# Kernel tuning notes

Measured on AMD Instinct MI355X. Metric: run time of the kernel, lower is better.

Reference implementation:

```python
import jax, jax.numpy as jnp
import numpy as np

NUM_LEVELS = 3
NUM_EMBEDDINGS = 1024
EMBEDDING_DIM = 128
COMMITMENT_COST = 0.25
N_TOKENS = 262144


def setup_inputs() -> dict:
    key = jax.random.key(0)
    k1, k2 = jax.random.split(key)
    z_e = jax.random.normal(k1, (N_TOKENS, EMBEDDING_DIM), dtype=jnp.float32)
    codebooks = jax.random.normal(k2, (NUM_LEVELS, NUM_EMBEDDINGS, EMBEDDING_DIM), dtype=jnp.float32)
    return {"z_e": z_e, "codebooks": codebooks}


def _rvq_forward(z_e, codebooks):
    """Sequential residual VQ: per level cdist + argmin + gather + residual update.

    Per-level losses follow the standard EMA-VQ formulation:
      vq_loss     = mean((z_q - sg(residual))^2)
      commit_loss = beta * mean((sg(z_q) - residual)^2)
    with straight-through estimator z_q_st = residual + sg(z_q - residual).
    """
    sg = jax.lax.stop_gradient
    residual = z_e
    z_q_total = jnp.zeros_like(z_e)
    all_indices = []
    vq_loss = jnp.float32(0.0)
    commit_loss = jnp.float32(0.0)
    num_levels = codebooks.shape[0]
    for lvl in range(num_levels):  # small fixed loop over levels (sequential by design)
        E = codebooks[lvl]  # [K, D]
        # squared-distance matrix [N, K]: ||r||^2 + ||e||^2 - 2 r.e
        d = (jnp.sum(residual * residual, axis=1, keepdims=True)
             + jnp.sum(E * E, axis=1)
             - 2.0 * (residual @ E.T))
        idx = jnp.argmin(d, axis=1)           # [N]
        z_q = E[idx]                           # gather [N, D]
        vq_loss = vq_loss + jnp.mean((z_q - sg(residual)) ** 2)
        commit_loss = commit_loss + COMMITMENT_COST * jnp.mean((sg(z_q) - residual) ** 2)
        z_q_st = residual + sg(z_q - residual)  # straight-through
        z_q_total = z_q_total + z_q_st
        residual = residual - z_q_st
        all_indices.append(idx)
    L = jnp.float32(num_levels)
    stacked_indices = jnp.stack(all_indices, axis=1)  # [N, num_levels]
    return z_q_total, vq_loss / L, commit_loss / L, stacked_indices


def reference(z_e, codebooks):
    return _rvq_forward(z_e, codebooks)
```

## Files before the change

### kernel.cpp

```cpp
#include <hip/hip_runtime.h>
#include <math.h>

#define N_TOK   262144
#define DIMV    128
#define KCODE   1024
#define LEV     3
#define BLOCK   256
#define NTILES  64
#define EPS     0.08f

#define WS_EE64_B  64
#define WS_EE32_B  24640
#define WS_FRAG_B  36928

typedef _Float16 f16x8 __attribute__((ext_vector_type(8)));
typedef float f32x4 __attribute__((ext_vector_type(4)));

__global__ void rvq_prep(const float* __restrict__ cb, double* __restrict__ ws) {
    int c = blockIdx.x * blockDim.x + threadIdx.x;
    if (c == 0) ws[0] = 0.0;
    if (c >= LEV * KCODE) return;
    const float* e = cb + (size_t)c * DIMV;
    const int lvl = c >> 10, ci = c & 1023, t4 = ci >> 4, n = ci & 15;
    unsigned char* fb = (unsigned char*)ws + WS_FRAG_B + (((size_t)(lvl * 64 + t4)) << 12);
    double s = 0.0;
    #pragma unroll
    for (int st = 0; st < 4; ++st)
        #pragma unroll
        for (int kq = 0; kq < 4; ++kq) {
            float4 a = *(const float4*)(e + st*32 + kq*8);
            float4 b = *(const float4*)(e + st*32 + kq*8 + 4);
            f16x8 h;
            h[0]=(_Float16)a.x; h[1]=(_Float16)a.y; h[2]=(_Float16)a.z; h[3]=(_Float16)a.w;
            h[4]=(_Float16)b.x; h[5]=(_Float16)b.y; h[6]=(_Float16)b.z; h[7]=(_Float16)b.w;
            s = fma((double)a.x,(double)a.x,s); s = fma((double)a.y,(double)a.y,s);
            s = fma((double)a.z,(double)a.z,s); s = fma((double)a.w,(double)a.w,s);
            s = fma((double)b.x,(double)b.x,s); s = fma((double)b.y,(double)b.y,s);
            s = fma((double)b.z,(double)b.z,s); s = fma((double)b.w,(double)b.w,s);
            *(f16x8*)(fb + st*1024 + ((kq*16 + n) << 4)) = h;
        }
    ((double*)((unsigned char*)ws + WS_EE64_B))[c] = s;
    ((float*)((unsigned char*)ws + WS_EE32_B))[c] = (float)(s + 8192.0);
}

__device__ inline unsigned sel4(const unsigned v[4], int j) {
    unsigned a = (j & 1) ? v[1] : v[0];
    unsigned b = (j & 1) ? v[3] : v[2];
    return (j & 2) ? b : a;
}

__global__ __launch_bounds__(BLOCK, 2) void rvq_main(const float* __restrict__ ze,
                                                     const float* __restrict__ cb,
                                                     float* __restrict__ out,
                                                     double* __restrict__ ws) {
    __shared__ double ssum[4];

    const double* __restrict__ ee64g = (const double*)((const unsigned char*)ws + WS_EE64_B);
    const float*  __restrict__ eebg  = (const float*)((const unsigned char*)ws + WS_EE32_B);
    const unsigned char* __restrict__ fbase = (const unsigned char*)ws + WS_FRAG_B;

    const int tid  = threadIdx.x;
    const int lane = tid & 63;
    const int wid  = tid >> 6;
    const int q    = lane >> 4;
    const int col  = lane & 15;
    const long tokbase = (long)blockIdx.x * 128 + wid * 32;

    float r[2][4][8];
    f16x8 Ah[2][4], Al[2][4];

    #pragma unroll
    for (int mt = 0; mt < 2; ++mt) {
        const float4* zp = (const float4*)(ze + (size_t)(tokbase + mt*16 + col) * DIMV);
        #pragma unroll
        for (int st = 0; st < 4; ++st) {
            float4 a = zp[st*8 + q*2], b = zp[st*8 + q*2 + 1];
            r[mt][st][0]=a.x; r[mt][st][1]=a.y; r[mt][st][2]=a.z; r[mt][st][3]=a.w;
            r[mt][st][4]=b.x; r[mt][st][5]=b.y; r[mt][st][6]=b.z; r[mt][st][7]=b.w;
        }
    }
    #pragma unroll
    for (int mt = 0; mt < 2; ++mt)
        #pragma unroll
        for (int st = 0; st < 4; ++st) {
            f16x8 h, lo;
            #pragma unroll
            for (int j = 0; j < 8; ++j) {
                float y = -2.0f * r[mt][st][j];
                _Float16 hh = (_Float16)y;
                h[j] = hh;
                lo[j] = (_Float16)(y - (float)hh);
            }
            Ah[mt][st] = h; Al[mt][st] = lo;
        }

    double loss = 0.0;
    float* out_idx = out + (size_t)N_TOK * DIMV + 2;

#define TILE_COMPUTE(B, EEQ, T)                                                      \
    do {                                                                             \
        f32x4 c0  = {(EEQ),(EEQ),(EEQ),(EEQ)};                                       \
        f32x4 c1v = {(EEQ),(EEQ),(EEQ),(EEQ)};                                       \
        c0  = __builtin_amdgcn_mfma_f32_16x16x32_f16(Ah[0][0], (B)[0], c0,  0,0,0);  \
        c1v = __builtin_amdgcn_mfma_f32_16x16x32_f16(Ah[1][0], (B)[0], c1v, 0,0,0);  \
        c0  = __builtin_amdgcn_mfma_f32_16x16x32_f16(Al[0][0], (B)[0], c0,  0,0,0);  \
        c1v = __builtin_amdgcn_mfma_f32_16x16x32_f16(Al[1][0], (B)[0], c1v, 0,0,0);  \
        c0  = __builtin_amdgcn_mfma_f32_16x16x32_f16(Ah[0][1], (B)[1], c0,  0,0,0);  \
        c1v = __builtin_amdgcn_mfma_f32_16x16x32_f16(Ah[1][1], (B)[1], c1v, 0,0,0);  \
        c0  = __builtin_amdgcn_mfma_f32_16x16x32_f16(Al[0][1], (B)[1], c0,  0,0,0);  \
        c1v = __builtin_amdgcn_mfma_f32_16x16x32_f16(Al[1][1], (B)[1], c1v, 0,0,0);  \
        c0  = __builtin_amdgcn_mfma_f32_16x16x32_f16(Ah[0][2], (B)[2], c0,  0,0,0);  \
        c1v = __builtin_amdgcn_mfma_f32_16x16x32_f16(Ah[1][2], (B)[2], c1v, 0,0,0);  \
        c0  = __builtin_amdgcn_mfma_f32_16x16x32_f16(Al[0][2], (B)[2], c0,  0,0,0);  \
        c1v = __builtin_amdgcn_mfma_f32_16x16x32_f16(Al[1][2], (B)[2], c1v, 0,0,0);  \
        c0  = __builtin_amdgcn_mfma_f32_16x16x32_f16(Ah[0][3], (B)[3], c0,  0,0,0);  \
        c1v = __builtin_amdgcn_mfma_f32_16x16x32_f16(Ah[1][3], (B)[3], c1v, 0,0,0);  \
        c0  = __builtin_amdgcn_mfma_f32_16x16x32_f16(Al[0][3], (B)[3], c0,  0,0,0);  \
        c1v = __builtin_amdgcn_mfma_f32_16x16x32_f16(Al[1][3], (B)[3], c1v, 0,0,0);  \
        _Pragma("unroll")                                                            \
        for (int i = 0; i < 4; ++i) {                                                \
            unsigned k0 = (__float_as_uint(c0[i]) << 6) | (unsigned)(T);             \
            m2[0][i] = min(m2[0][i], max(m1[0][i], k0));                             \
            m1[0][i] = min(m1[0][i], k0);                                            \
            unsigned k1_ = (__float_as_uint(c1v[i]) << 6) | (unsigned)(T);           \
            m2[1][i] = min(m2[1][i], max(m1[1][i], k1_));                            \
            m1[1][i] = min(m1[1][i], k1_);                                           \
        }                                                                            \
    } while (0)

    for (int l = 0; l < LEV; ++l) {
        const unsigned char* bp = fbase + ((size_t)l << 18) + (lane << 4);
        const float* eep = eebg + l * KCODE + col;

        f16x8 Ba[4], Bb[4];
        #pragma unroll
        for (int st = 0; st < 4; ++st) Ba[st] = *(const f16x8*)(bp + st*1024);
        float eeq_a = eep[0], eeq_b;

        unsigned m1[2][4], m2[2][4];
        #pragma unroll
        for (int mt = 0; mt < 2; ++mt)
            #pragma unroll
            for (int i = 0; i < 4; ++i) { m1[mt][i] = 0xFFFFFFFFu; m2[mt][i] = 0xFFFFFFFFu; }

        for (int t = 0; t < NTILES; t += 2) {
            {
                const unsigned char* np = bp + 4096;
                #pragma unroll
                for (int st = 0; st < 4; ++st) Bb[st] = *(const f16x8*)(np + st*1024);
                eeq_b = eep[16];
            }
            TILE_COMPUTE(Ba, eeq_a, t);
            {
                const unsigned char* np = (t + 2 < NTILES) ? bp + 8192 : bp;
                const float* ep2 = (t + 2 < NTILES) ? eep + 32 : eep;
                #pragma unroll
                for (int st = 0; st < 4; ++st) Ba[st] = *(const f16x8*)(np + st*1024);
                eeq_a = ep2[0];
            }
            TILE_COMPUTE(Bb, eeq_b, t + 1);
            bp += 8192; eep += 32;
        }

        unsigned k1[2][4], k2[2][4], q1[2][4], q2[2][4];
        #pragma unroll
        for (int mt = 0; mt < 2; ++mt)
            #pragma unroll
            for (int i = 0; i < 4; ++i) {
                k1[mt][i] = m1[mt][i]; k2[mt][i] = m2[mt][i];
                q1[mt][i] = (unsigned)col; q2[mt][i] = (unsigned)col;
            }
        #pragma unroll
        for (int d = 1; d <= 8; d <<= 1) {
            #pragma unroll
            for (int mt = 0; mt < 2; ++mt)
                #pragma unroll
                for (int i = 0; i < 4; ++i) {
                    unsigned ok1 = __shfl_xor(k1[mt][i], d), oq1 = __shfl_xor(q1[mt][i], d);
                    unsigned ok2 = __shfl_xor(k2[mt][i], d), oq2 = __shfl_xor(q2[mt][i], d);
                    bool sw = (ok1 < k1[mt][i]) || (ok1 == k1[mt][i] && oq1 < q1[mt][i]);
                    unsigned n1 = sw ? ok1 : k1[mt][i], nq1 = sw ? oq1 : q1[mt][i];
                    unsigned hk = sw ? k1[mt][i] : ok1, hq = sw ? q1[mt][i] : oq1;
                    bool s2 = (ok2 < k2[mt][i]) || (ok2 == k2[mt][i] && oq2 < q2[mt][i]);
                    unsigned p2 = s2 ? ok2 : k2[mt][i], pq = s2 ? oq2 : q2[mt][i];
                    bool s3 = (p2 < hk) || (p2 == hk && pq < hq);
                    k1[mt][i] = n1;              q1[mt][i] = nq1;
                    k2[mt][i] = s3 ? p2 : hk;    q2[mt][i] = s3 ? pq : hq;
                }
        }

        int jsel = (lane >> 2) & 3;
        int S = ((col >> 2) << 4) | ((col & 3) << 2);

        #pragma unroll
        for (int mt = 0; mt < 2; ++mt) {
            unsigned sk1 = sel4(k1[mt], jsel), sq1 = sel4(q1[mt], jsel);
            unsigned sk2 = sel4(k2[mt], jsel), sq2 = sel4(q2[mt], jsel);
            unsigned bk1 = (unsigned)__shfl((int)sk1, S);
            unsigned bq1 = (unsigned)__shfl((int)sq1, S);
            unsigned bk2 = (unsigned)__shfl((int)sk2, S);
            unsigned bq2 = (unsigned)__shfl((int)sq2, S);
            int c1c = (int)(((bk1 & 63u) << 4) | bq1);
            int c2c = (int)(((bk2 & 63u) << 4) | bq2);
            float d1 = __uint_as_float((bk1 >> 6) | 0x44000000u) - 8192.0f;
            float d2 = __uint_as_float((bk2 >> 6) | 0x44000000u) - 8192.0f;
            int bc = c1c;
            if (d2 - d1 < EPS) {
                double s1 = 0.0, s2d = 0.0;
                const float4* e1 = (const float4*)(cb + ((size_t)l*KCODE + c1c)*DIMV);
                const float4* e2 = (const float4*)(cb + ((size_t)l*KCODE + c2c)*DIMV);
                #pragma unroll
                for (int st = 0; st < 4; ++st) {
                    float4 a = e1[st*8 + q*2], b = e1[st*8 + q*2 + 1];
                    s1 = fma((double)a.x,(double)r[mt][st][0],s1); s1 = fma((double)a.y,(double)r[mt][st][1],s1);
                    s1 = fma((double)a.z,(double)r[mt][st][2],s1); s1 = fma((double)a.w,(double)r[mt][st][3],s1);
                    s1 = fma((double)b.x,(double)r[mt][st][4],s1); s1 = fma((double)b.y,(double)r[mt][st][5],s1);
                    s1 = fma((double)b.z,(double)r[mt][st][6],s1); s1 = fma((double)b.w,(double)r[mt][st][7],s1);
                    float4 a2 = e2[st*8 + q*2], b2 = e2[st*8 + q*2 + 1];
                    s2d = fma((double)a2.x,(double)r[mt][st][0],s2d); s2d = fma((double)a2.y,(double)r[mt][st][1],s2d);
                    s2d = fma((double)a2.z,(double)r[mt][st][2],s2d); s2d = fma((double)a2.w,(double)r[mt][st][3],s2d);
                    s2d = fma((double)b2.x,(double)r[mt][st][4],s2d); s2d = fma((double)b2.y,(double)r[mt][st][5],s2d);
                    s2d = fma((double)b2.z,(double)r[mt][st][6],s2d); s2d = fma((double)b2.w,(double)r[mt][st][7],s2d);
                }
                s1  += __shfl_xor(s1, 16);  s1  += __shfl_xor(s1, 32);
                s2d += __shfl_xor(s2d, 16); s2d += __shfl_xor(s2d, 32);
                double dd1 = ee64g[l*KCODE + c1c] - 2.0*s1;
                double dd2 = ee64g[l*KCODE + c2c] - 2.0*s2d;
                if (dd2 < dd1 || (dd2 == dd1 && c2c < c1c)) bc = c2c;
            }
            const float4* eb = (const float4*)(cb + ((size_t)l*KCODE + bc)*DIMV);
            #pragma unroll
            for (int st = 0; st < 4; ++st) {
                float4 a = eb[st*8 + q*2], b = eb[st*8 + q*2 + 1];
                float qv[8] = {a.x,a.y,a.z,a.w,b.x,b.y,b.z,b.w};
                #pragma unroll
                for (int j = 0; j < 8; ++j) {
                    float rv = r[mt][st][j];
                    float t1 = qv[j] - rv;
                    loss += (double)t1 * (double)t1;
                    float zqst = rv + t1;
                    r[mt][st][j] = rv - zqst;
                }
            }
            if (l < LEV - 1) {
                #pragma unroll
                for (int st = 0; st < 4; ++st) {
                    f16x8 h, lo;
                    #pragma unroll
                    for (int j = 0; j < 8; ++j) {
                        float y = -2.0f * r[mt][st][j];
                        _Float16 hh = (_Float16)y;
                        h[j] = hh;
                        lo[j] = (_Float16)(y - (float)hh);
                    }
                    Ah[mt][st] = h; Al[mt][st] = lo;
                }
            } else {
                const float4* zp = (const float4*)(ze + (size_t)(tokbase + mt*16 + col)*DIMV);
                float4* op = (float4*)(out + (size_t)(tokbase + mt*16 + col)*DIMV);
                #pragma unroll
                for (int st = 0; st < 4; ++st) {
                    float4 za = zp[st*8 + q*2], zb = zp[st*8 + q*2 + 1];
                    float4 oa, ob;
                    oa.x = za.x - r[mt][st][0]; oa.y = za.y - r[mt][st][1];
                    oa.z = za.z - r[mt][st][2]; oa.w = za.w - r[mt][st][3];
                    ob.x = zb.x - r[mt][st][4]; ob.y = zb.y - r[mt][st][5];
                    ob.z = zb.z - r[mt][st][6]; ob.w = zb.w - r[mt][st][7];
                    op[st*8 + q*2] = oa; op[st*8 + q*2 + 1] = ob;
                }
            }
            if (q == 0) out_idx[(size_t)(tokbase + mt*16 + col)*3 + l] = (float)bc;
        }
    }

    #pragma unroll
    for (int d = 1; d <= 32; d <<= 1) loss += __shfl_xor(loss, d);
    if ((tid & 63) == 0) ssum[wid] = loss;
    __syncthreads();
    if (tid == 0) atomicAdd(ws, ssum[0] + ssum[1] + ssum[2] + ssum[3]);
}

__global__ void rvq_fin(const double* __restrict__ ws, float* __restrict__ out) {
    double vq = ws[0] / ((double)N_TOK * (double)DIMV * (double)LEV);
    out[(size_t)N_TOK * DIMV + 0] = (float)vq;
    out[(size_t)N_TOK * DIMV + 1] = (float)(0.25 * vq);
}

extern "C" void kernel_launch(void* const* d_in, const int* in_sizes, int n_in,
                              void* d_out, int out_size, void* d_ws, size_t ws_size,
                              hipStream_t stream) {
    const float* ze = (const float*)d_in[0];
    const float* cb = (const float*)d_in[1];
    float* out = (float*)d_out;
    double* ws = (double*)d_ws;

    rvq_prep<<<(LEV * KCODE + 255) / 256, 256, 0, stream>>>(cb, ws);
    rvq_main<<<N_TOK / 128, BLOCK, 0, stream>>>(ze, cb, out, ws);
    rvq_fin<<<1, 1, 0, stream>>>(ws, out);
}
```

Measured before the change: 733.9 us.

## Recompute residual from input and chosen codes instead of holding it in registers

The per-thread fp32 residual array is dropped. At each level the residual is rebuilt by reloading z_e and replaying the earlier levels' chosen codebook rows, which frees registers so launch bounds can go from 2 to 3 blocks per SM. The top-2 tracking uses v_med3_u32 in place of min/max, and the residual update, fp16 split and output write are merged into one loop. The cost is extra global and cache reads of z_e and codebook rows at every level.

```diff
diff --git a/kernel.cpp b/kernel.cpp
--- a/kernel.cpp
+++ b/kernel.cpp
@@ -49,7 +49,44 @@
     return (j & 2) ? b : a;
 }
 
-__global__ __launch_bounds__(BLOCK, 2) void rvq_main(const float* __restrict__ ze,
+__device__ inline unsigned umed3(unsigned a, unsigned b, unsigned c) {
+    unsigned d;
+    asm("v_med3_u32 %0, %1, %2, %3" : "=v"(d) : "v"(a), "v"(b), "v"(c));
+    return d;
+}
+
+#define REPLAY_CHUNK(ZP, ST, ZZ, RR, MT)                                              \
+    do {                                                                              \
+        float4 za_ = (ZP)[(ST)*8 + q*2], zb_ = (ZP)[(ST)*8 + q*2 + 1];                \
+        ZZ[0]=za_.x; ZZ[1]=za_.y; ZZ[2]=za_.z; ZZ[3]=za_.w;                           \
+        ZZ[4]=zb_.x; ZZ[5]=zb_.y; ZZ[6]=zb_.z; ZZ[7]=zb_.w;                           \
+        _Pragma("unroll")                                                             \
+        for (int j_ = 0; j_ < 8; ++j_) RR[j_] = ZZ[j_];                               \
+        if (l > 0) {                                                                  \
+            const float4* ep_ = (const float4*)(cb + (size_t)pb[MT][0]*DIMV);         \
+            float4 ea_ = ep_[(ST)*8 + q*2], eb_ = ep_[(ST)*8 + q*2 + 1];              \
+            float ev_[8] = {ea_.x,ea_.y,ea_.z,ea_.w,eb_.x,eb_.y,eb_.z,eb_.w};         \
+            _Pragma("unroll")                                                         \
+            for (int j_ = 0; j_ < 8; ++j_) {                                          \
+                float t1_ = ev_[j_] - RR[j_];                                         \
+                float zq_ = RR[j_] + t1_;                                             \
+                RR[j_] = RR[j_] - zq_;                                                \
+            }                                                                         \
+        }                                                                             \
+        if (l > 1) {                                                                  \
+            const float4* ep_ = (const float4*)(cb + (size_t)(KCODE + pb[MT][1])*DIMV); \
+            float4 ea_ = ep_[(ST)*8 + q*2], eb_ = ep_[(ST)*8 + q*2 + 1];              \
+            float ev_[8] = {ea_.x,ea_.y,ea_.z,ea_.w,eb_.x,eb_.y,eb_.z,eb_.w};         \
+            _Pragma("unroll")                                                         \
+            for (int j_ = 0; j_ < 8; ++j_) {                                          \
+                float t1_ = ev_[j_] - RR[j_];                                         \
+                float zq_ = RR[j_] + t1_;                                             \
+                RR[j_] = RR[j_] - zq_;                                                \
+            }                                                                         \
+        }                                                                             \
+    } while (0)
+
+__global__ __launch_bounds__(BLOCK, 3) void rvq_main(const float* __restrict__ ze,
                                                      const float* __restrict__ cb,
                                                      float* __restrict__ out,
                                                      double* __restrict__ ws) {
@@ -66,8 +103,8 @@
     const int col  = lane & 15;
     const long tokbase = (long)blockIdx.x * 128 + wid * 32;
 
-    float r[2][4][8];
     f16x8 Ah[2][4], Al[2][4];
+    int pb[2][2];
 
     #pragma unroll
     for (int mt = 0; mt < 2; ++mt) {
@@ -75,24 +112,18 @@
         #pragma unroll
         for (int st = 0; st < 4; ++st) {
             float4 a = zp[st*8 + q*2], b = zp[st*8 + q*2 + 1];
-            r[mt][st][0]=a.x; r[mt][st][1]=a.y; r[mt][st][2]=a.z; r[mt][st][3]=a.w;
-            r[mt][st][4]=b.x; r[mt][st][5]=b.y; r[mt][st][6]=b.z; r[mt][st][7]=b.w;
-        }
-    }
-    #pragma unroll
-    for (int mt = 0; mt < 2; ++mt)
-        #pragma unroll
-        for (int st = 0; st < 4; ++st) {
+            float rv[8] = {a.x,a.y,a.z,a.w,b.x,b.y,b.z,b.w};
             f16x8 h, lo;
             #pragma unroll
             for (int j = 0; j < 8; ++j) {
-                float y = -2.0f * r[mt][st][j];
+                float y = -2.0f * rv[j];
                 _Float16 hh = (_Float16)y;
                 h[j] = hh;
                 lo[j] = (_Float16)(y - (float)hh);
             }
             Ah[mt][st] = h; Al[mt][st] = lo;
         }
+    }
 
     double loss = 0.0;
     float* out_idx = out + (size_t)N_TOK * DIMV + 2;
@@ -120,10 +151,10 @@
         _Pragma("unroll")                                                            \
         for (int i = 0; i < 4; ++i) {                                                \
             unsigned k0 = (__float_as_uint(c0[i]) << 6) | (unsigned)(T);             \
-            m2[0][i] = min(m2[0][i], max(m1[0][i], k0));                             \
+            m2[0][i] = umed3(m1[0][i], m2[0][i], k0);                                \
             m1[0][i] = min(m1[0][i], k0);                                            \
             unsigned k1_ = (__float_as_uint(c1v[i]) << 6) | (unsigned)(T);           \
-            m2[1][i] = min(m2[1][i], max(m1[1][i], k1_));                            \
+            m2[1][i] = umed3(m1[1][i], m2[1][i], k1_);                               \
             m1[1][i] = min(m1[1][i], k1_);                                           \
         }                                                                            \
     } while (0)
@@ -205,22 +236,25 @@
             float d1 = __uint_as_float((bk1 >> 6) | 0x44000000u) - 8192.0f;
             float d2 = __uint_as_float((bk2 >> 6) | 0x44000000u) - 8192.0f;
             int bc = c1c;
+            const float4* zp2 = (const float4*)(ze + (size_t)(tokbase + mt*16 + col)*DIMV);
             if (d2 - d1 < EPS) {
                 double s1 = 0.0, s2d = 0.0;
                 const float4* e1 = (const float4*)(cb + ((size_t)l*KCODE + c1c)*DIMV);
                 const float4* e2 = (const float4*)(cb + ((size_t)l*KCODE + c2c)*DIMV);
                 #pragma unroll
                 for (int st = 0; st < 4; ++st) {
+                    float rr[8], zz[8];
+                    REPLAY_CHUNK(zp2, st, zz, rr, mt);
                     float4 a = e1[st*8 + q*2], b = e1[st*8 + q*2 + 1];
-                    s1 = fma((double)a.x,(double)r[mt][st][0],s1); s1 = fma((double)a.y,(double)r[mt][st][1],s1);
-                    s1 = fma((double)a.z,(double)r[mt][st][2],s1); s1 = fma((double)a.w,(double)r[mt][st][3],s1);
-                    s1 = fma((double)b.x,(double)r[mt][st][4],s1); s1 = fma((double)b.y,(double)r[mt][st][5],s1);
-                    s1 = fma((double)b.z,(double)r[mt][st][6],s1); s1 = fma((double)b.w,(double)r[mt][st][7],s1);
+                    s1 = fma((double)a.x,(double)rr[0],s1); s1 = fma((double)a.y,(double)rr[1],s1);
+                    s1 = fma((double)a.z,(double)rr[2],s1); s1 = fma((double)a.w,(double)rr[3],s1);
+                    s1 = fma((double)b.x,(double)rr[4],s1); s1 = fma((double)b.y,(double)rr[5],s1);
+                    s1 = fma((double)b.z,(double)rr[6],s1); s1 = fma((double)b.w,(double)rr[7],s1);
                     float4 a2 = e2[st*8 + q*2], b2 = e2[st*8 + q*2 + 1];
-                    s2d = fma((double)a2.x,(double)r[mt][st][0],s2d); s2d = fma((double)a2.y,(double)r[mt][st][1],s2d);
-                    s2d = fma((double)a2.z,(double)r[mt][st][2],s2d); s2d = fma((double)a2.w,(double)r[mt][st][3],s2d);
-                    s2d = fma((double)b2.x,(double)r[mt][st][4],s2d); s2d = fma((double)b2.y,(double)r[mt][st][5],s2d);
-                    s2d = fma((double)b2.z,(double)r[mt][st][6],s2d); s2d = fma((double)b2.w,(double)r[mt][st][7],s2d);
+                    s2d = fma((double)a2.x,(double)rr[0],s2d); s2d = fma((double)a2.y,(double)rr[1],s2d);
+                    s2d = fma((double)a2.z,(double)rr[2],s2d); s2d = fma((double)a2.w,(double)rr[3],s2d);
+                    s2d = fma((double)b2.x,(double)rr[4],s2d); s2d = fma((double)b2.y,(double)rr[5],s2d);
+                    s2d = fma((double)b2.z,(double)rr[6],s2d); s2d = fma((double)b2.w,(double)rr[7],s2d);
                 }
                 s1  += __shfl_xor(s1, 16);  s1  += __shfl_xor(s1, 32);
                 s2d += __shfl_xor(s2d, 16); s2d += __shfl_xor(s2d, 32);
@@ -228,47 +262,38 @@
                 double dd2 = ee64g[l*KCODE + c2c] - 2.0*s2d;
                 if (dd2 < dd1 || (dd2 == dd1 && c2c < c1c)) bc = c2c;
             }
-            const float4* eb = (const float4*)(cb + ((size_t)l*KCODE + bc)*DIMV);
+            const float4* ebp = (const float4*)(cb + ((size_t)l*KCODE + bc)*DIMV);
+            float4* op = (float4*)(out + (size_t)(tokbase + mt*16 + col)*DIMV);
             #pragma unroll
             for (int st = 0; st < 4; ++st) {
-                float4 a = eb[st*8 + q*2], b = eb[st*8 + q*2 + 1];
+                float rr[8], zz[8];
+                REPLAY_CHUNK(zp2, st, zz, rr, mt);
+                float4 a = ebp[st*8 + q*2], b = ebp[st*8 + q*2 + 1];
                 float qv[8] = {a.x,a.y,a.z,a.w,b.x,b.y,b.z,b.w};
+                f16x8 h, lo;
+                float ov[8];
                 #pragma unroll
                 for (int j = 0; j < 8; ++j) {
-                    float rv = r[mt][st][j];
+                    float rv = rr[j];
                     float t1 = qv[j] - rv;
                     loss += (double)t1 * (double)t1;
                     float zqst = rv + t1;
-                    r[mt][st][j] = rv - zqst;
+                    float rn = rv - zqst;
+                    float y = -2.0f * rn;
+                    _Float16 hh = (_Float16)y;
+                    h[j] = hh;
+                    lo[j] = (_Float16)(y - (float)hh);
+                    ov[j] = zz[j] - rn;
                 }
-            }
-            if (l < LEV - 1) {
-                #pragma unroll
-                for (int st = 0; st < 4; ++st) {
-                    f16x8 h, lo;
-                    #pragma unroll
-                    for (int j = 0; j < 8; ++j) {
-                        float y = -2.0f * r[mt][st][j];
-                        _Float16 hh = (_Float16)y;
-                        h[j] = hh;
-                        lo[j] = (_Float16)(y - (float)hh);
-                    }
-                    Ah[mt][st] = h; Al[mt][st] = lo;
-                }
-            } else {
-                const float4* zp = (const float4*)(ze + (size_t)(tokbase + mt*16 + col)*DIMV);
-                float4* op = (float4*)(out + (size_t)(tokbase + mt*16 + col)*DIMV);
-                #pragma unroll
-                for (int st = 0; st < 4; ++st) {
-                    float4 za = zp[st*8 + q*2], zb = zp[st*8 + q*2 + 1];
-                    float4 oa, ob;
-                    oa.x = za.x - r[mt][st][0]; oa.y = za.y - r[mt][st][1];
-                    oa.z = za.z - r[mt][st][2]; oa.w = za.w - r[mt][st][3];
-                    ob.x = zb.x - r[mt][st][4]; ob.y = zb.y - r[mt][st][5];
-                    ob.z = zb.z - r[mt][st][6]; ob.w = zb.w - r[mt][st][7];
+                if (l < LEV - 1) { Ah[mt][st] = h; Al[mt][st] = lo; }
+                else {
+                    float4 oa = {ov[0],ov[1],ov[2],ov[3]};
+                    float4 ob = {ov[4],ov[5],ov[6],ov[7]};
                     op[st*8 + q*2] = oa; op[st*8 + q*2 + 1] = ob;
                 }
             }
+            if (l == 0) pb[mt][0] = bc;
+            if (l == 1) pb[mt][1] = bc;
             if (q == 0) out_idx[(size_t)(tokbase + mt*16 + col)*3 + l] = (float)bc;
         }
     }
```

Measured after the change: 784.7 us. 1.07x slower.

## Stream codebook tiles through per-wave LDS ring via async global_load_lds

Applied to the files above, without the earlier changes.

Codebook fragment tiles are no longer loaded directly into registers. Each wave now streams them into its own 4-slot LDS ring with global_load_lds, prefetching three tiles ahead, and synchronises with explicit vmcnt waits. The per-level codebook norms are staged in shared memory, and the top-2 tracking uses v_med3_u32 instead of min/max. This is meant to hide global memory latency behind the MFMA work. In exchange it uses 64KB+ of LDS per block, which may cut occupancy below the two blocks requested, and hand-written waitcnt counting is fragile.

```diff
diff --git a/kernel.cpp b/kernel.cpp
--- a/kernel.cpp
+++ b/kernel.cpp
@@ -7,6 +7,7 @@
 #define LEV     3
 #define BLOCK   256
 #define NTILES  64
+#define RDEPTH  4
 #define EPS     0.08f
 
 #define WS_EE64_B  64
@@ -49,10 +50,29 @@
     return (j & 2) ? b : a;
 }
 
+__device__ inline unsigned umed3(unsigned a, unsigned b, unsigned c) {
+    unsigned d;
+    asm("v_med3_u32 %0, %1, %2, %3" : "=v"(d) : "v"(a), "v"(b), "v"(c));
+    return d;
+}
+
+__device__ inline void dma_tile(const unsigned char* g, unsigned char* l) {
+    #pragma unroll
+    for (int st = 0; st < 4; ++st)
+        __builtin_amdgcn_global_load_lds(
+            (const __attribute__((address_space(1))) void*)(g + st*1024),
+            (__attribute__((address_space(3))) void*)(l + st*1024),
+            16, 0, 0);
+}
+
+#define WAITV(N) asm volatile("s_waitcnt vmcnt(" #N ")" ::: "memory")
+
 __global__ __launch_bounds__(BLOCK, 2) void rvq_main(const float* __restrict__ ze,
                                                      const float* __restrict__ cb,
                                                      float* __restrict__ out,
                                                      double* __restrict__ ws) {
+    __shared__ __align__(16) unsigned char Bring[4 * RDEPTH * 4096];
+    __shared__ __align__(16) float eeS[KCODE];
     __shared__ double ssum[4];
 
     const double* __restrict__ ee64g = (const double*)((const unsigned char*)ws + WS_EE64_B);
@@ -65,6 +85,8 @@
     const int q    = lane >> 4;
     const int col  = lane & 15;
     const long tokbase = (long)blockIdx.x * 128 + wid * 32;
+
+    unsigned char* ring = Bring + (size_t)wid * (RDEPTH * 4096);
 
     float r[2][4][8];
     f16x8 Ah[2][4], Al[2][4];
@@ -120,22 +142,35 @@
         _Pragma("unroll")                                                            \
         for (int i = 0; i < 4; ++i) {                                                \
             unsigned k0 = (__float_as_uint(c0[i]) << 6) | (unsigned)(T);             \
-            m2[0][i] = min(m2[0][i], max(m1[0][i], k0));                             \
+            m2[0][i] = umed3(m1[0][i], m2[0][i], k0);                                \
             m1[0][i] = min(m1[0][i], k0);                                            \
             unsigned k1_ = (__float_as_uint(c1v[i]) << 6) | (unsigned)(T);           \
-            m2[1][i] = min(m2[1][i], max(m1[1][i], k1_));                            \
+            m2[1][i] = umed3(m1[1][i], m2[1][i], k1_);                               \
             m1[1][i] = min(m1[1][i], k1_);                                           \
         }                                                                            \
     } while (0)
 
+#define READB(DST, SLOT)                                                             \
+    do {                                                                             \
+        const unsigned char* sb_ = ring + (SLOT) * 4096 + (lane << 4);               \
+        _Pragma("unroll")                                                            \
+        for (int st = 0; st < 4; ++st) DST[st] = *(const f16x8*)(sb_ + st*1024);     \
+    } while (0)
+
     for (int l = 0; l < LEV; ++l) {
-        const unsigned char* bp = fbase + ((size_t)l << 18) + (lane << 4);
-        const float* eep = eebg + l * KCODE + col;
-
+        __syncthreads();
+        ((float4*)eeS)[tid] = ((const float4*)(eebg + (size_t)l * KCODE))[tid];
+        __syncthreads();
+
+        const unsigned char* ft = fbase + ((size_t)l << 18) + (lane << 4);
+
+        WAITV(0);
+        #pragma unroll
+        for (int p = 0; p < 3; ++p) dma_tile(ft + p*4096, ring + p*4096);
+        WAITV(8);
         f16x8 Ba[4], Bb[4];
-        #pragma unroll
-        for (int st = 0; st < 4; ++st) Ba[st] = *(const f16x8*)(bp + st*1024);
-        float eeq_a = eep[0], eeq_b;
+        READB(Ba, 0);
+        float eeq_a = eeS[col], eeq_b;
 
         unsigned m1[2][4], m2[2][4];
         #pragma unroll
@@ -144,22 +179,26 @@
             for (int i = 0; i < 4; ++i) { m1[mt][i] = 0xFFFFFFFFu; m2[mt][i] = 0xFFFFFFFFu; }
 
         for (int t = 0; t < NTILES; t += 2) {
-            {
-                const unsigned char* np = bp + 4096;
-                #pragma unroll
-                for (int st = 0; st < 4; ++st) Bb[st] = *(const f16x8*)(np + st*1024);
-                eeq_b = eep[16];
-            }
+            if (t + 3 < NTILES) {
+                dma_tile(ft + (size_t)(t+3)*4096, ring + ((t+3)&3)*4096);
+                WAITV(8);
+            } else {
+                WAITV(0);
+            }
+            READB(Bb, (t+1)&3);
+            eeq_b = eeS[(t+1)*16 + col];
             TILE_COMPUTE(Ba, eeq_a, t);
-            {
-                const unsigned char* np = (t + 2 < NTILES) ? bp + 8192 : bp;
-                const float* ep2 = (t + 2 < NTILES) ? eep + 32 : eep;
-                #pragma unroll
-                for (int st = 0; st < 4; ++st) Ba[st] = *(const f16x8*)(np + st*1024);
-                eeq_a = ep2[0];
+            if (t + 4 < NTILES) {
+                dma_tile(ft + (size_t)(t+4)*4096, ring + ((t+4)&3)*4096);
+                WAITV(8);
+                READB(Ba, (t+2)&3);
+                eeq_a = eeS[(t+2)*16 + col];
+            } else if (t + 2 < NTILES) {
+                WAITV(4);
+                READB(Ba, (t+2)&3);
+                eeq_a = eeS[(t+2)*16 + col];
             }
             TILE_COMPUTE(Bb, eeq_b, t + 1);
-            bp += 8192; eep += 32;
         }
 
         unsigned k1[2][4], k2[2][4], q1[2][4], q2[2][4];
```

Measured after the change: 717.9 us. 2.2% less time.
